# Performance work log

Hardware: AMD Instinct MI355X
Metric: run time of the kernel (lower is better)

The kernel has to match this reference:

```python
import jax, jax.numpy as jnp
import numpy as np
from math import sqrt

B, S, F, H, FF, L = 16, 512, 512, 8, 2048, 3
HEAD_DIM = F // H
LN_EPS = 1e-5


def setup_inputs() -> dict:
    key = jax.random.key(0)
    ks = iter(jax.random.split(key, 80))

    def nrm(shape, scale=0.02):
        return jax.random.normal(next(ks), shape, jnp.float32) * scale

    inp = {
        "embedding": jax.random.normal(next(ks), (B, S, F), jnp.float32),
        "lengths": jax.random.randint(next(ks), (B,), 1, S + 1, dtype=jnp.int32),
    }
    for p in ("enc", "dec"):
        inp[p + "_wqkv"] = nrm((L, 3, F, F))
        inp[p + "_bqkv"] = nrm((L, 3, F))
        inp[p + "_wo"] = nrm((L, F, F))
        inp[p + "_bo"] = nrm((L, F))
        inp[p + "_ln1_g"] = jnp.ones((L, F), jnp.float32)
        inp[p + "_ln1_b"] = jnp.zeros((L, F), jnp.float32)
        inp[p + "_ff_w1"] = nrm((L, F, FF))
        inp[p + "_ff_b1"] = nrm((L, FF))
        inp[p + "_ff_w2"] = nrm((L, FF, F))
        inp[p + "_ff_b2"] = nrm((L, F))
        inp[p + "_ln2_g"] = jnp.ones((L, F), jnp.float32)
        inp[p + "_ln2_b"] = jnp.zeros((L, F), jnp.float32)
    inp["ptr_w_q"] = nrm((F,), 1.0)
    inp["ptr_w_k"] = nrm((F,), 1.0)
    return inp


def _ln(x, g, b):
    mu = x.mean(-1, keepdims=True)
    var = ((x - mu) ** 2).mean(-1, keepdims=True)
    return (x - mu) / jnp.sqrt(var + LN_EPS) * g + b


def _mha(q_in, kv_in, wqkv, bqkv, wo, bo, mask):
    # q_in [b,sq,f], kv_in [b,sk,f], mask broadcastable to [b,h,sq,sk] (True = masked)
    b, sq, f = q_in.shape
    q = q_in @ wqkv[0] + bqkv[0]
    k = kv_in @ wqkv[1] + bqkv[1]
    v = kv_in @ wqkv[2] + bqkv[2]

    def split(t):
        return t.reshape(t.shape[0], t.shape[1], H, HEAD_DIM).transpose(0, 2, 1, 3)

    q, k, v = split(q), split(k), split(v)  # [b,h,s,dh]
    scores = jnp.einsum("bhqd,bhkd->bhqk", q, k) / sqrt(HEAD_DIM)
    scores = jnp.where(mask, jnp.finfo(scores.dtype).min, scores)
    attn = jax.nn.softmax(scores, axis=-1)
    out = jnp.einsum("bhqk,bhkd->bhqd", attn, v)
    out = out.transpose(0, 2, 1, 3).reshape(b, sq, f)
    return out @ wo + bo


def _layer(x, mem, mask, wqkv, bqkv, wo, bo, ln1_g, ln1_b, w1, b1, w2, b2, ln2_g, ln2_b):
    x = _ln(x + _mha(x, mem, wqkv, bqkv, wo, bo, mask), ln1_g, ln1_b)
    ff = jax.nn.gelu(x @ w1 + b1, approximate=False) @ w2 + b2
    return _ln(x + ff, ln2_g, ln2_b)


def _forward(embedding, lengths,
             enc_wqkv, enc_bqkv, enc_wo, enc_bo, enc_ln1_g, enc_ln1_b,
             enc_ff_w1, enc_ff_b1, enc_ff_w2, enc_ff_b2, enc_ln2_g, enc_ln2_b,
             dec_wqkv, dec_bqkv, dec_wo, dec_bo, dec_ln1_g, dec_ln1_b,
             dec_ff_w1, dec_ff_b1, dec_ff_w2, dec_ff_b2, dec_ln2_g, dec_ln2_b,
             ptr_w_q, ptr_w_k):
    b, s, f = embedding.shape
    pos = jnp.arange(s)
    key_mask = pos[None, :] >= lengths[:, None]  # [b,s] True = padded

    # ---- encoder (self-attn with key padding mask) ----
    enc_mask = key_mask[:, None, None, :]  # [b,1,1,s]
    x = embedding
    for i in range(L):
        x = _layer(x, x, enc_mask,
                   enc_wqkv[i], enc_bqkv[i], enc_wo[i], enc_bo[i],
                   enc_ln1_g[i], enc_ln1_b[i],
                   enc_ff_w1[i], enc_ff_b1[i], enc_ff_w2[i], enc_ff_b2[i],
                   enc_ln2_g[i], enc_ln2_b[i])
    memory = x

    # ---- decoder: all timesteps batched (no recurrent state in original loop) ----
    # query t attends keys j < min(t, len); t=0 is overridden with zeros below
    # (key 0 left unmasked for t=0 only to keep softmax finite).
    t = jnp.arange(s)
    limit = jnp.minimum(jnp.maximum(t, 1)[None, :], lengths[:, None])  # [b,sq]
    dec_mask = (pos[None, None, :] >= limit[:, :, None])[:, None, :, :]  # [b,1,sq,sk]
    y = embedding
    for i in range(L):
        y = _layer(y, memory, dec_mask,
                   dec_wqkv[i], dec_bqkv[i], dec_wo[i], dec_bo[i],
                   dec_ln1_g[i], dec_ln1_b[i],
                   dec_ff_w1[i], dec_ff_b1[i], dec_ff_w2[i], dec_ff_b2[i],
                   dec_ln2_g[i], dec_ln2_b[i])

    # ---- pointer logits ----
    wq = y @ ptr_w_q        # [b, sq]
    wk = memory @ ptr_w_k   # [b, sk]
    ptr = jax.nn.sigmoid((wq[:, None, :] + wk[:, :, None]) / sqrt(f))  # [b, sk, sq]
    return jnp.where(t[None, None, :] == 0, 0.0, ptr)


def reference(embedding, lengths,
              enc_wqkv, enc_bqkv, enc_wo, enc_bo, enc_ln1_g, enc_ln1_b,
              enc_ff_w1, enc_ff_b1, enc_ff_w2, enc_ff_b2, enc_ln2_g, enc_ln2_b,
              dec_wqkv, dec_bqkv, dec_wo, dec_bo, dec_ln1_g, dec_ln1_b,
              dec_ff_w1, dec_ff_b1, dec_ff_w2, dec_ff_b2, dec_ln2_g, dec_ln2_b,
              ptr_w_q, ptr_w_k):
    return _forward(embedding, lengths,
                    enc_wqkv, enc_bqkv, enc_wo, enc_bo, enc_ln1_g, enc_ln1_b,
                    enc_ff_w1, enc_ff_b1, enc_ff_w2, enc_ff_b2, enc_ln2_g, enc_ln2_b,
                    dec_wqkv, dec_bqkv, dec_wo, dec_bo, dec_ln1_g, dec_ln1_b,
                    dec_ff_w1, dec_ff_b1, dec_ff_w2, dec_ff_b2, dec_ln2_g, dec_ln2_b,
                    ptr_w_q, ptr_w_k)
```

## Files before the change

kernel.cpp:

```cpp
#include <hip/hip_runtime.h>
#include <hip/hip_bf16.h>
#include <math.h>

#define TB 16
#define TS 512
#define TF 512
#define TH 8
#define TFF 2048
#define TL 3

typedef unsigned short u16;
typedef short bf16x8 __attribute__((ext_vector_type(8)));
typedef float f32x4 __attribute__((ext_vector_type(4)));

__device__ __forceinline__ u16 f2b(float f) {
    __hip_bfloat16 h = __float2bfloat16(f);
    return *reinterpret_cast<u16*>(&h);
}

__device__ __forceinline__ void gload_lds16(const void* g, void* l) {
    __builtin_amdgcn_global_load_lds(
        (const __attribute__((address_space(1))) unsigned int*)g,
        (__attribute__((address_space(3))) unsigned int*)l, 16, 0, 0);
}

__global__ __launch_bounds__(256) void k_transpose_w(
    const float* __restrict__ src, u16* __restrict__ dst, int K, int N)
{
    __shared__ float tile[32][33];
    const int z = blockIdx.z;
    src += (size_t)z * K * N;
    dst += (size_t)z * K * N;
    const int n0 = blockIdx.x * 32, k0 = blockIdx.y * 32;
    const int tx = threadIdx.x & 31, ty = threadIdx.x >> 5;
    #pragma unroll
    for (int i = 0; i < 32; i += 8)
        tile[ty + i][tx] = src[(size_t)(k0 + ty + i) * N + n0 + tx];
    __syncthreads();
    #pragma unroll
    for (int i = 0; i < 32; i += 8)
        dst[(size_t)(n0 + ty + i) * K + k0 + tx] = f2b(tile[tx][ty + i]);
}

__global__ __launch_bounds__(256) void k_cvt(
    const float* __restrict__ src, float* __restrict__ d32,
    u16* __restrict__ d16, int n4)
{
    const int i = blockIdx.x * 256 + threadIdx.x;
    if (i >= n4) return;
    float4 v = ((const float4*)src)[i];
    if (d32) ((float4*)d32)[i] = v;
    ushort4 p;
    p.x = f2b(v.x); p.y = f2b(v.y); p.z = f2b(v.z); p.w = f2b(v.w);
    ((ushort4*)d16)[i] = p;
}

template<int EPI, int BN>
__global__ __launch_bounds__(512, 1) void k_g8(
    const u16* __restrict__ A, const u16* __restrict__ A2, int asplit,
    const u16* __restrict__ BT,
    const float* __restrict__ bias, const float* __restrict__ resid,
    u16* __restrict__ outb, float* __restrict__ outf,
    u16* __restrict__ out_k, u16* __restrict__ out_v,
    int N, int K, int ldo, int coloff)
{
    constexpr int NFB = BN / 64;
    constexpr int NL = 2 + BN / 64;
    __shared__ __align__(16) u16 SH[2 * 128 * 64 + 2 * BN * 64];
    u16* Asm = SH;
    u16* Bsm = SH + 2 * 128 * 64;

    const int gx = gridDim.x;
    int bid = blockIdx.y * gx + blockIdx.x;
    const int cpx = (gx * gridDim.y) >> 3;
    bid = (bid & 7) * cpx + (bid >> 3);
    const int bn = bid % gx, bm = bid / gx;

    const int t = threadIdx.x;
    const int w = t >> 6, l = t & 63;
    const int wm = w >> 2, wn = w & 3;
    const int lhi = l >> 4, llo = l & 15;

    f32x4 acc[4][NFB];
    #pragma unroll
    for (int m = 0; m < 4; ++m)
        #pragma unroll
        for (int n = 0; n < NFB; ++n)
            acc[m][n] = f32x4{0.f, 0.f, 0.f, 0.f};

    const u16* Asrc = (bn * BN < asplit) ? A : A2;
    const int lr = l >> 3;
    const int lcz = ((l & 7) ^ lr) * 8;
    const u16* Ag = Asrc + (size_t)(bm * 128 + w * 8 + lr) * K + lcz;
    const u16* Bg = BT + (size_t)(bn * BN + w * 8 + lr) * K + lcz;

    auto stage = [&](int buf, int tt) {
        const int kofs = tt << 6;
        gload_lds16(Ag + kofs,          Asm + buf * 8192 + (w * 8) * 64);
        gload_lds16(Ag + 64 * K + kofs, Asm + buf * 8192 + (64 + w * 8) * 64);
        #pragma unroll
        for (int i = 0; i < BN / 64; ++i)
            gload_lds16(Bg + (size_t)i * 64 * K + kofs,
                        Bsm + buf * (BN * 64) + (i * 64 + w * 8) * 64);
    };

    const int NT = K >> 6;
    stage(0, 0);
    stage(1, 1);
    for (int tt = 0; tt < NT; ++tt) {
        const int cur = tt & 1;
        if (tt + 1 < NT) {
            if constexpr (BN == 256) asm volatile("s_waitcnt vmcnt(6)" ::: "memory");
            else                     asm volatile("s_waitcnt vmcnt(4)" ::: "memory");
        } else {
            asm volatile("s_waitcnt vmcnt(0)" ::: "memory");
        }
        __builtin_amdgcn_s_barrier();
        __builtin_amdgcn_sched_barrier(0);

        bf16x8 af[4][2], bfr[NFB][2];
        #pragma unroll
        for (int m = 0; m < 4; ++m) {
            const int row = wm * 64 + m * 16 + llo;
            const int x = row & 7;
            af[m][0] = *(const bf16x8*)(Asm + cur * 8192 + row * 64 + ((lhi) ^ x) * 8);
            af[m][1] = *(const bf16x8*)(Asm + cur * 8192 + row * 64 + ((4 + lhi) ^ x) * 8);
        }
        #pragma unroll
        for (int n = 0; n < NFB; ++n) {
            const int row = wn * (BN / 4) + n * 16 + llo;
            const int x = row & 7;
            bfr[n][0] = *(const bf16x8*)(Bsm + cur * (BN * 64) + row * 64 + ((lhi) ^ x) * 8);
            bfr[n][1] = *(const bf16x8*)(Bsm + cur * (BN * 64) + row * 64 + ((4 + lhi) ^ x) * 8);
        }
        asm volatile("s_waitcnt lgkmcnt(0)" ::: "memory");
        __builtin_amdgcn_sched_barrier(0);
        __builtin_amdgcn_s_setprio(1);
        #pragma unroll
        for (int m = 0; m < 2; ++m)
            #pragma unroll
            for (int n = 0; n < NFB; ++n) {
                acc[m][n] = __builtin_amdgcn_mfma_f32_16x16x32_bf16(af[m][0], bfr[n][0], acc[m][n], 0, 0, 0);
                acc[m][n] = __builtin_amdgcn_mfma_f32_16x16x32_bf16(af[m][1], bfr[n][1], acc[m][n], 0, 0, 0);
            }
        __builtin_amdgcn_s_setprio(0);
        __builtin_amdgcn_sched_barrier(0);
        __builtin_amdgcn_s_barrier();
        if (tt + 2 < NT) stage(cur, tt + 2);
        __builtin_amdgcn_s_setprio(1);
        #pragma unroll
        for (int m = 2; m < 4; ++m)
            #pragma unroll
            for (int n = 0; n < NFB; ++n) {
                acc[m][n] = __builtin_amdgcn_mfma_f32_16x16x32_bf16(af[m][0], bfr[n][0], acc[m][n], 0, 0, 0);
                acc[m][n] = __builtin_amdgcn_mfma_f32_16x16x32_bf16(af[m][1], bfr[n][1], acc[m][n], 0, 0, 0);
            }
        __builtin_amdgcn_s_setprio(0);
    }

    const int colb = bn * BN + wn * (BN / 4);
    const int rowb = bm * 128 + wm * 64 + lhi * 4;
    const int c0w = coloff + colb;

    if constexpr (EPI == 3 && BN == 256) {
        if (c0w >= 1024) {
            u16* tb = SH + w * 4096;
            #pragma unroll
            for (int n = 0; n < 4; ++n) {
                const int dl = n * 16 + llo;
                const float bv = bias[colb + n * 16 + llo];
                #pragma unroll
                for (int m = 0; m < 4; ++m) {
                    ushort4 pk;
                    #pragma unroll
                    for (int r = 0; r < 4; ++r)
                        ((u16*)&pk)[r] = f2b(acc[m][n][r] + bv);
                    const int slc = m * 2 + (lhi >> 1);
                    const int addr = dl * 64 + ((slc ^ (dl & 7)) << 3) + ((lhi & 1) << 2);
                    *(ushort4*)(tb + addr) = pk;
                }
            }
            asm volatile("s_waitcnt lgkmcnt(0)" ::: "memory");
            __builtin_amdgcn_sched_barrier(0);
            const int sbase = bm * 128 + wm * 64;
            const int bidx = sbase >> 9;
            const int srem = sbase & 511;
            const int hh = (c0w >> 6) & 7;
            u16* vo = out_v + ((size_t)bidx * 8 + hh) * 32768 + srem;
            const int cchunk = l & 7;
            #pragma unroll
            for (int rr = 0; rr < 8; ++rr) {
                const int dl2 = (l >> 3) + rr * 8;
                const int ch = cchunk ^ (dl2 & 7);
                bf16x8 vv = *(const bf16x8*)(tb + dl2 * 64 + ch * 8);
                *(bf16x8*)(vo + (size_t)dl2 * 512 + cchunk * 8) = vv;
            }
            return;
        }
    }

    #pragma unroll
    for (int n = 0; n < NFB; ++n) {
        const int col = colb + n * 16 + llo;
        const float bv = bias[col];
        #pragma unroll
        for (int m = 0; m < 4; ++m) {
            const int row = rowb + m * 16;
            if (EPI == 3) {
                float vv[4];
                #pragma unroll
                for (int r = 0; r < 4; ++r) vv[r] = acc[m][n][r] + bv;
                const int c = coloff + col;
                if ((c >> 9) == 0) {
                    #pragma unroll
                    for (int r = 0; r < 4; ++r)
                        outb[(size_t)(row + r) * 512 + c] = f2b(vv[r]);
                } else {
                    const int hh = (c >> 6) & 7, d = c & 63;
                    #pragma unroll
                    for (int r = 0; r < 4; ++r) {
                        const int rr = row + r;
                        out_k[((size_t)(rr >> 9) * 8 + hh) * 32768 + (rr & 511) * 64 + d] = f2b(vv[r]);
                    }
                }
            } else {
                #pragma unroll
                for (int r = 0; r < 4; ++r) {
                    float v = acc[m][n][r] + bv;
                    const size_t off = (size_t)(row + r) * ldo + coloff + col;
                    if (EPI == 0) {
                        outb[off] = f2b(v);
                    } else if (EPI == 1) {
                        v = 0.5f * v * (1.f + erff(v * 0.70710678118654752f));
                        outb[off] = f2b(v);
                    } else {
                        outf[off] = v + resid[off];
                    }
                }
            }
        }
    }
}

template<int DEC>
__global__ __launch_bounds__(256) void k_attn(
    const u16* __restrict__ qb, const u16* __restrict__ kc,
    const u16* __restrict__ vtp, const int* __restrict__ lengths,
    u16* __restrict__ out)
{
    __shared__ __align__(16) u16 Ks[2][64 * 64];
    __shared__ __align__(16) u16 Vs[2][64 * 64];
    __shared__ __align__(16) u16 plds[4][16][64];
    __shared__ float alds[4][16];
    __shared__ float llds[4][16];
    const int qt = blockIdx.x;
    const int bh = blockIdx.y;
    const int b = bh >> 3;
    const int h = bh & 7;
    const int t = threadIdx.x, w = t >> 6, l = t & 63;
    const int lhi = l >> 4, llo = l & 15;
    const int len = lengths[b];
    const int qrow0 = qt * 64 + w * 16;
    const int q = qrow0 + llo;

    const u16* qp = qb + (size_t)(b * TS + q) * 512 + h * 64 + lhi * 8;
    bf16x8 qf0 = *(const bf16x8*)(qp);
    bf16x8 qf1 = *(const bf16x8*)(qp + 32);

    const u16* kb = kc  + (size_t)bh * 32768;
    const u16* vb = vtp + (size_t)bh * 32768;

    const int qlim = DEC ? min(max(q, 1), len) : len;
    const int limb = DEC ? min(qt * 64 + 63, len) : len;
    const int ktend = (limb + 63) >> 6;

    f32x4 o[4];
    #pragma unroll
    for (int g = 0; g < 4; ++g) o[g] = f32x4{0.f, 0.f, 0.f, 0.f};
    float mrun = -1e30f, lrun = 0.f;

    const float SC = 0.18033688011112042f;

    const int sr = w * 8 + (l >> 3);
    const int sc = (((l & 7) ^ (sr & 7)) << 3);
    auto stage = [&](int buf, int ktt) {
        gload_lds16(kb + ((ktt * 64 + sr) << 6) + sc,        &Ks[buf][(w * 8) * 64]);
        gload_lds16(kb + ((ktt * 64 + 32 + sr) << 6) + sc,   &Ks[buf][(32 + w * 8) * 64]);
        gload_lds16(vb + (size_t)sr * 512 + ktt * 64 + sc,   &Vs[buf][(w * 8) * 64]);
        gload_lds16(vb + (size_t)(32 + sr) * 512 + ktt * 64 + sc, &Vs[buf][(32 + w * 8) * 64]);
    };

    stage(0, 0);
    for (int kt = 0; kt < ktend; ++kt) {
        const int cur = kt & 1;
        if (kt + 1 < ktend) {
            stage(cur ^ 1, kt + 1);
            asm volatile("s_waitcnt vmcnt(4)" ::: "memory");
        } else {
            asm volatile("s_waitcnt vmcnt(0)" ::: "memory");
        }
        __builtin_amdgcn_s_barrier();
        __builtin_amdgcn_sched_barrier(0);

        bf16x8 kf[4][2], vf[4][2];
        #pragma unroll
        for (int g = 0; g < 4; ++g) {
            const int row = g * 16 + llo;
            const int x = row & 7;
            kf[g][0] = *(const bf16x8*)&Ks[cur][row * 64 + ((lhi) ^ x) * 8];
            kf[g][1] = *(const bf16x8*)&Ks[cur][row * 64 + ((4 + lhi) ^ x) * 8];
            vf[g][0] = *(const bf16x8*)&Vs[cur][row * 64 + ((lhi) ^ x) * 8];
            vf[g][1] = *(const bf16x8*)&Vs[cur][row * 64 + ((4 + lhi) ^ x) * 8];
        }
        f32x4 s[4];
        #pragma unroll
        for (int g = 0; g < 4; ++g) {
            s[g] = f32x4{0.f, 0.f, 0.f, 0.f};
            s[g] = __builtin_amdgcn_mfma_f32_16x16x32_bf16(kf[g][0], qf0, s[g], 0, 0, 0);
            s[g] = __builtin_amdgcn_mfma_f32_16x16x32_bf16(kf[g][1], qf1, s[g], 0, 0, 0);
        }
        #pragma unroll
        for (int g = 0; g < 4; ++g) {
            const int key = kt * 64 + g * 16 + lhi * 4;
            #pragma unroll
            for (int r = 0; r < 4; ++r)
                s[g][r] = (key + r < qlim) ? s[g][r] * SC : -1e30f;
        }
        float tm = fmaxf(fmaxf(fmaxf(s[0][0], s[0][1]), fmaxf(s[0][2], s[0][3])),
                         fmaxf(fmaxf(s[1][0], s[1][1]), fmaxf(s[1][2], s[1][3])));
        tm = fmaxf(tm, fmaxf(fmaxf(fmaxf(s[2][0], s[2][1]), fmaxf(s[2][2], s[2][3])),
                             fmaxf(fmaxf(s[3][0], s[3][1]), fmaxf(s[3][2], s[3][3]))));
        tm = fmaxf(tm, __shfl_xor(tm, 16));
        tm = fmaxf(tm, __shfl_xor(tm, 32));
        const float mnew = fmaxf(mrun, tm);
        const float alpha = exp2f(mrun - mnew);
        mrun = mnew;
        float rs = 0.f;
        ushort4 pk[4];
        #pragma unroll
        for (int g = 0; g < 4; ++g) {
            #pragma unroll
            for (int r = 0; r < 4; ++r) {
                const float p = exp2f(s[g][r] - mnew);
                rs += p;
                ((u16*)&pk[g])[r] = f2b(p);
            }
        }
        rs += __shfl_xor(rs, 16);
        rs += __shfl_xor(rs, 32);
        lrun = lrun * alpha + rs;
        if (lhi == 0) alds[w][llo] = alpha;
        #pragma unroll
        for (int g = 0; g < 4; ++g) {
            const int chw = (g * 2 + (lhi >> 1)) ^ (llo & 7);
            *(ushort4*)((char*)&plds[w][0][0] + llo * 128 + chw * 16 + (lhi & 1) * 8) = pk[g];
        }
        const float4 av = *(const float4*)&alds[w][lhi * 4];
        #pragma unroll
        for (int g = 0; g < 4; ++g) {
            o[g][0] *= av.x; o[g][1] *= av.y; o[g][2] *= av.z; o[g][3] *= av.w;
        }
        #pragma unroll
        for (int ks = 0; ks < 2; ++ks) {
            const int chr = (ks * 4 + lhi) ^ (llo & 7);
            bf16x8 pa = *(const bf16x8*)((const char*)&plds[w][0][0] + llo * 128 + chr * 16);
            #pragma unroll
            for (int g = 0; g < 4; ++g)
                o[g] = __builtin_amdgcn_mfma_f32_16x16x32_bf16(pa, vf[g][ks], o[g], 0, 0, 0);
        }
        __builtin_amdgcn_sched_barrier(0);
        __builtin_amdgcn_s_barrier();
    }

    if (lhi == 0) llds[w][llo] = 1.f / lrun;
    __builtin_amdgcn_s_waitcnt(0);
    const float4 linv = *(const float4*)&llds[w][lhi * 4];
    #pragma unroll
    for (int g = 0; g < 4; ++g) {
        const int d = h * 64 + g * 16 + llo;
        #pragma unroll
        for (int r = 0; r < 4; ++r) {
            const int qq = qrow0 + lhi * 4 + r;
            out[(size_t)(b * TS + qq) * 512 + d] = f2b(o[g][r] * ((const float*)&linv)[r]);
        }
    }
}

__global__ __launch_bounds__(256) void k_ln(
    const float* __restrict__ in, const float* __restrict__ gam,
    const float* __restrict__ bet, float* __restrict__ o32, u16* __restrict__ o16)
{
    const int row = blockIdx.x * 4 + (threadIdx.x >> 6);
    const int l = threadIdx.x & 63;
    const float* p = in + (size_t)row * 512 + l * 8;
    float x[8];
    *(float4*)&x[0] = *(const float4*)p;
    *(float4*)&x[4] = *(const float4*)(p + 4);
    float s = x[0] + x[1] + x[2] + x[3] + x[4] + x[5] + x[6] + x[7];
    #pragma unroll
    for (int off = 32; off; off >>= 1) s += __shfl_xor(s, off);
    const float mu = s * (1.f / 512.f);
    float v = 0.f;
    #pragma unroll
    for (int i = 0; i < 8; ++i) { const float d = x[i] - mu; v += d * d; }
    #pragma unroll
    for (int off = 32; off; off >>= 1) v += __shfl_xor(v, off);
    const float rstd = rsqrtf(v * (1.f / 512.f) + 1e-5f);
    float gg[8], bb[8];
    *(float4*)&gg[0] = *(const float4*)(gam + l * 8);
    *(float4*)&gg[4] = *(const float4*)(gam + l * 8 + 4);
    *(float4*)&bb[0] = *(const float4*)(bet + l * 8);
    *(float4*)&bb[4] = *(const float4*)(bet + l * 8 + 4);
    float y[8];
    #pragma unroll
    for (int i = 0; i < 8; ++i) y[i] = (x[i] - mu) * rstd * gg[i] + bb[i];
    float* op = o32 + (size_t)row * 512 + l * 8;
    *(float4*)op = *(float4*)&y[0];
    *(float4*)(op + 4) = *(float4*)&y[4];
    ushort4 pk0, pk1;
    pk0.x = f2b(y[0]); pk0.y = f2b(y[1]); pk0.z = f2b(y[2]); pk0.w = f2b(y[3]);
    pk1.x = f2b(y[4]); pk1.y = f2b(y[5]); pk1.z = f2b(y[6]); pk1.w = f2b(y[7]);
    ushort4* o16p = (ushort4*)(o16 + (size_t)row * 512 + l * 8);
    o16p[0] = pk0; o16p[1] = pk1;
}

__global__ __launch_bounds__(256) void k_rowdot(
    const float* __restrict__ x, const float* __restrict__ wv, float* __restrict__ out)
{
    const int row = blockIdx.x * 4 + (threadIdx.x >> 6);
    const int l = threadIdx.x & 63;
    const float* p = x + (size_t)row * 512 + l * 8;
    float4 a = *(const float4*)p;
    float4 b = *(const float4*)(p + 4);
    float4 wa = *(const float4*)(wv + l * 8);
    float4 wb = *(const float4*)(wv + l * 8 + 4);
    float s = a.x * wa.x + a.y * wa.y + a.z * wa.z + a.w * wa.w
            + b.x * wb.x + b.y * wb.y + b.z * wb.z + b.w * wb.w;
    #pragma unroll
    for (int off = 32; off; off >>= 1) s += __shfl_xor(s, off);
    if (l == 0) out[row] = s;
}

__global__ __launch_bounds__(256) void k_ptr_out(
    const float* __restrict__ wq, const float* __restrict__ wk, float* __restrict__ out)
{
    const int bi = blockIdx.x;
    const int b = bi >> 9;
    const float wki = wk[bi];
    #pragma unroll
    for (int j = threadIdx.x; j < 512; j += 256) {
        float r = 0.f;
        if (j != 0) {
            const float z = (wq[b * 512 + j] + wki) * 0.044194173824159216f;
            r = 1.f / (1.f + __expf(-z));
        }
        out[(size_t)bi * 512 + j] = r;
    }
}

extern "C" void kernel_launch(void* const* d_in, const int* in_sizes, int n_in,
                              void* d_out, int out_size, void* d_ws, size_t ws_size,
                              hipStream_t stream)
{
    const float* emb = (const float*)d_in[0];
    const int* lengths = (const int*)d_in[1];
    struct Pw {
        const float *wqkv, *bqkv, *wo, *bo, *ln1g, *ln1b, *w1, *b1, *w2, *b2, *ln2g, *ln2b;
    } pp[2];
    for (int p = 0; p < 2; ++p) {
        const int base = 2 + p * 12;
        pp[p].wqkv = (const float*)d_in[base + 0];
        pp[p].bqkv = (const float*)d_in[base + 1];
        pp[p].wo   = (const float*)d_in[base + 2];
        pp[p].bo   = (const float*)d_in[base + 3];
        pp[p].ln1g = (const float*)d_in[base + 4];
        pp[p].ln1b = (const float*)d_in[base + 5];
        pp[p].w1   = (const float*)d_in[base + 6];
        pp[p].b1   = (const float*)d_in[base + 7];
        pp[p].w2   = (const float*)d_in[base + 8];
        pp[p].b2   = (const float*)d_in[base + 9];
        pp[p].ln2g = (const float*)d_in[base + 10];
        pp[p].ln2b = (const float*)d_in[base + 11];
    }
    const float* pwq = (const float*)d_in[26];
    const float* pwk = (const float*)d_in[27];

    char* ws = (char*)d_ws;
    auto alloc = [&](size_t bytes) {
        char* p = ws;
        ws += (bytes + 255) & ~(size_t)255;
        return p;
    };
    u16* wqkvT[2], *woT[2], *w1T[2], *w2T[2];
    for (int p = 0; p < 2; ++p) {
        wqkvT[p] = (u16*)alloc((size_t)TL * 1536 * 512 * 2);
        woT[p]   = (u16*)alloc((size_t)TL * 512 * 512 * 2);
        w1T[p]   = (u16*)alloc((size_t)TL * 2048 * 512 * 2);
        w2T[p]   = (u16*)alloc((size_t)TL * 512 * 2048 * 2);
    }
    const size_t MR = (size_t)TB * TS;
    float* x32   = (float*)alloc(MR * 512 * 4);
    u16*   x16   = (u16*)alloc(MR * 512 * 2);
    float* mem32 = (float*)alloc(MR * 512 * 4);
    u16*   mem16 = (u16*)alloc(MR * 512 * 2);
    u16*   qbuf  = (u16*)alloc(MR * 512 * 2);
    u16*   kcb   = (u16*)alloc((size_t)TB * TH * 512 * 64 * 2);
    u16*   vtb   = (u16*)alloc((size_t)TB * TH * 64 * 512 * 2);
    u16*   att16 = (u16*)alloc(MR * 512 * 2);
    float* preln = (float*)alloc(MR * 512 * 4);
    u16*   h16   = (u16*)alloc(MR * 2048 * 2);
    float* wqb   = (float*)alloc(MR * 4);
    float* wkb   = (float*)alloc(MR * 4);

    for (int p = 0; p < 2; ++p) {
        k_transpose_w<<<dim3(16, 16, 9), 256, 0, stream>>>(pp[p].wqkv, wqkvT[p], 512, 512);
        k_transpose_w<<<dim3(16, 16, 3), 256, 0, stream>>>(pp[p].wo, woT[p], 512, 512);
        k_transpose_w<<<dim3(64, 16, 3), 256, 0, stream>>>(pp[p].w1, w1T[p], 512, 2048);
        k_transpose_w<<<dim3(16, 64, 3), 256, 0, stream>>>(pp[p].w2, w2T[p], 2048, 512);
    }

    const int n4 = (int)(MR * 512 / 4);
    k_cvt<<<4096, 256, 0, stream>>>(emb, x32, x16, n4);

    for (int i = 0; i < TL; ++i) {
        k_g8<3, 256><<<dim3(6, 64), 512, 0, stream>>>(
            x16, x16, 1536, wqkvT[0] + (size_t)i * 1536 * 512, pp[0].bqkv + i * 1536,
            nullptr, qbuf, nullptr, kcb, vtb, 1536, 512, 1536, 0);
        k_attn<0><<<dim3(8, 128), 256, 0, stream>>>(qbuf, kcb, vtb, lengths, att16);
        k_g8<2, 128><<<dim3(4, 64), 512, 0, stream>>>(
            att16, att16, 512, woT[0] + (size_t)i * 512 * 512, pp[0].bo + i * 512,
            x32, nullptr, preln, nullptr, nullptr, 512, 512, 512, 0);
        k_ln<<<2048, 256, 0, stream>>>(preln, pp[0].ln1g + i * 512, pp[0].ln1b + i * 512, x32, x16);
        k_g8<1, 256><<<dim3(8, 64), 512, 0, stream>>>(
            x16, x16, 2048, w1T[0] + (size_t)i * 2048 * 512, pp[0].b1 + i * 2048,
            nullptr, h16, nullptr, nullptr, nullptr, 2048, 512, 2048, 0);
        k_g8<2, 128><<<dim3(4, 64), 512, 0, stream>>>(
            h16, h16, 512, w2T[0] + (size_t)i * 512 * 2048, pp[0].b2 + i * 512,
            x32, nullptr, preln, nullptr, nullptr, 512, 2048, 512, 0);
        if (i == TL - 1)
            k_ln<<<2048, 256, 0, stream>>>(preln, pp[0].ln2g + i * 512, pp[0].ln2b + i * 512, mem32, mem16);
        else
            k_ln<<<2048, 256, 0, stream>>>(preln, pp[0].ln2g + i * 512, pp[0].ln2b + i * 512, x32, x16);
    }
    k_cvt<<<4096, 256, 0, stream>>>(emb, x32, x16, n4);

    for (int i = 0; i < TL; ++i) {
        k_g8<3, 256><<<dim3(6, 64), 512, 0, stream>>>(
            x16, mem16, 512, wqkvT[1] + (size_t)i * 1536 * 512, pp[1].bqkv + i * 1536,
            nullptr, qbuf, nullptr, kcb, vtb, 1536, 512, 1536, 0);
        k_attn<1><<<dim3(8, 128), 256, 0, stream>>>(qbuf, kcb, vtb, lengths, att16);
        k_g8<2, 128><<<dim3(4, 64), 512, 0, stream>>>(
            att16, att16, 512, woT[1] + (size_t)i * 512 * 512, pp[1].bo + i * 512,
            x32, nullptr, preln, nullptr, nullptr, 512, 512, 512, 0);
        k_ln<<<2048, 256, 0, stream>>>(preln, pp[1].ln1g + i * 512, pp[1].ln1b + i * 512, x32, x16);
        k_g8<1, 256><<<dim3(8, 64), 512, 0, stream>>>(
            x16, x16, 2048, w1T[1] + (size_t)i * 2048 * 512, pp[1].b1 + i * 2048,
            nullptr, h16, nullptr, nullptr, nullptr, 2048, 512, 2048, 0);
        k_g8<2, 128><<<dim3(4, 64), 512, 0, stream>>>(
            h16, h16, 512, w2T[1] + (size_t)i * 512 * 2048, pp[1].b2 + i * 512,
            x32, nullptr, preln, nullptr, nullptr, 512, 2048, 512, 0);
        k_ln<<<2048, 256, 0, stream>>>(preln, pp[1].ln2g + i * 512, pp[1].ln2b + i * 512, x32, x16);
    }

    k_rowdot<<<2048, 256, 0, stream>>>(x32, pwq, wqb);
    k_rowdot<<<2048, 256, 0, stream>>>(mem32, pwk, wkb);
    k_ptr_out<<<TB * TS, 256, 0, stream>>>(wqb, wkb, (float*)d_out);
}
```

Before: 977.5 us.

## Keep residual stream in bf16 and fuse pointer row-dots into final layernorm

The fp32 residual copies (x32, mem32, preln) are removed. The residual add in the output GEMM epilogue now reads and writes bf16, and layernorm reads bf16 input and writes only bf16. The two pointer row-dot kernels are folded into the last layernorm of the encoder and decoder. This cuts memory traffic across the elementwise and epilogue stages and drops two launches, but the residual path and LN input now carry bf16 rounding error, which may affect accuracy.

After: 873.5 us. 10.6% less time.

```diff
diff --git a/kernel.cpp b/kernel.cpp
--- a/kernel.cpp
+++ b/kernel.cpp
@@ -17,6 +17,10 @@
     __hip_bfloat16 h = __float2bfloat16(f);
     return *reinterpret_cast<u16*>(&h);
 }
+__device__ __forceinline__ float b2f(u16 u) {
+    unsigned int v = ((unsigned int)u) << 16;
+    return __builtin_bit_cast(float, v);
+}
 
 __device__ __forceinline__ void gload_lds16(const void* g, void* l) {
     __builtin_amdgcn_global_load_lds(
@@ -43,13 +47,11 @@
 }
 
 __global__ __launch_bounds__(256) void k_cvt(
-    const float* __restrict__ src, float* __restrict__ d32,
-    u16* __restrict__ d16, int n4)
+    const float* __restrict__ src, u16* __restrict__ d16, int n4)
 {
     const int i = blockIdx.x * 256 + threadIdx.x;
     if (i >= n4) return;
     float4 v = ((const float4*)src)[i];
-    if (d32) ((float4*)d32)[i] = v;
     ushort4 p;
     p.x = f2b(v.x); p.y = f2b(v.y); p.z = f2b(v.z); p.w = f2b(v.w);
     ((ushort4*)d16)[i] = p;
@@ -59,13 +61,12 @@
 __global__ __launch_bounds__(512, 1) void k_g8(
     const u16* __restrict__ A, const u16* __restrict__ A2, int asplit,
     const u16* __restrict__ BT,
-    const float* __restrict__ bias, const float* __restrict__ resid,
-    u16* __restrict__ outb, float* __restrict__ outf,
+    const float* __restrict__ bias, const u16* __restrict__ residb,
+    u16* __restrict__ outb,
     u16* __restrict__ out_k, u16* __restrict__ out_v,
     int N, int K, int ldo, int coloff)
 {
     constexpr int NFB = BN / 64;
-    constexpr int NL = 2 + BN / 64;
     __shared__ __align__(16) u16 SH[2 * 128 * 64 + 2 * BN * 64];
     u16* Asm = SH;
     u16* Bsm = SH + 2 * 128 * 64;
@@ -234,7 +235,8 @@
                         v = 0.5f * v * (1.f + erff(v * 0.70710678118654752f));
                         outb[off] = f2b(v);
                     } else {
-                        outf[off] = v + resid[off];
+                        v += b2f(residb[off]);
+                        outb[off] = f2b(v);
                     }
                 }
             }
@@ -387,15 +389,16 @@
 }
 
 __global__ __launch_bounds__(256) void k_ln(
-    const float* __restrict__ in, const float* __restrict__ gam,
-    const float* __restrict__ bet, float* __restrict__ o32, u16* __restrict__ o16)
+    const u16* __restrict__ in, const float* __restrict__ gam,
+    const float* __restrict__ bet, u16* __restrict__ o16,
+    const float* __restrict__ dotv, float* __restrict__ dotout)
 {
     const int row = blockIdx.x * 4 + (threadIdx.x >> 6);
     const int l = threadIdx.x & 63;
-    const float* p = in + (size_t)row * 512 + l * 8;
+    bf16x8 vin = *(const bf16x8*)(in + (size_t)row * 512 + l * 8);
     float x[8];
-    *(float4*)&x[0] = *(const float4*)p;
-    *(float4*)&x[4] = *(const float4*)(p + 4);
+    #pragma unroll
+    for (int i = 0; i < 8; ++i) x[i] = b2f((u16)vin[i]);
     float s = x[0] + x[1] + x[2] + x[3] + x[4] + x[5] + x[6] + x[7];
     #pragma unroll
     for (int off = 32; off; off >>= 1) s += __shfl_xor(s, off);
@@ -414,31 +417,22 @@
     float y[8];
     #pragma unroll
     for (int i = 0; i < 8; ++i) y[i] = (x[i] - mu) * rstd * gg[i] + bb[i];
-    float* op = o32 + (size_t)row * 512 + l * 8;
-    *(float4*)op = *(float4*)&y[0];
-    *(float4*)(op + 4) = *(float4*)&y[4];
     ushort4 pk0, pk1;
     pk0.x = f2b(y[0]); pk0.y = f2b(y[1]); pk0.z = f2b(y[2]); pk0.w = f2b(y[3]);
     pk1.x = f2b(y[4]); pk1.y = f2b(y[5]); pk1.z = f2b(y[6]); pk1.w = f2b(y[7]);
     ushort4* o16p = (ushort4*)(o16 + (size_t)row * 512 + l * 8);
     o16p[0] = pk0; o16p[1] = pk1;
-}
-
-__global__ __launch_bounds__(256) void k_rowdot(
-    const float* __restrict__ x, const float* __restrict__ wv, float* __restrict__ out)
-{
-    const int row = blockIdx.x * 4 + (threadIdx.x >> 6);
-    const int l = threadIdx.x & 63;
-    const float* p = x + (size_t)row * 512 + l * 8;
-    float4 a = *(const float4*)p;
-    float4 b = *(const float4*)(p + 4);
-    float4 wa = *(const float4*)(wv + l * 8);
-    float4 wb = *(const float4*)(wv + l * 8 + 4);
-    float s = a.x * wa.x + a.y * wa.y + a.z * wa.z + a.w * wa.w
-            + b.x * wb.x + b.y * wb.y + b.z * wb.z + b.w * wb.w;
-    #pragma unroll
-    for (int off = 32; off; off >>= 1) s += __shfl_xor(s, off);
-    if (l == 0) out[row] = s;
+    if (dotv) {
+        float wa[8];
+        *(float4*)&wa[0] = *(const float4*)(dotv + l * 8);
+        *(float4*)&wa[4] = *(const float4*)(dotv + l * 8 + 4);
+        float ds = 0.f;
+        #pragma unroll
+        for (int i = 0; i < 8; ++i) ds += y[i] * wa[i];
+        #pragma unroll
+        for (int off = 32; off; off >>= 1) ds += __shfl_xor(ds, off);
+        if (l == 0) dotout[row] = ds;
+    }
 }
 
 __global__ __launch_bounds__(256) void k_ptr_out(
@@ -499,15 +493,13 @@
         w2T[p]   = (u16*)alloc((size_t)TL * 512 * 2048 * 2);
     }
     const size_t MR = (size_t)TB * TS;
-    float* x32   = (float*)alloc(MR * 512 * 4);
     u16*   x16   = (u16*)alloc(MR * 512 * 2);
-    float* mem32 = (float*)alloc(MR * 512 * 4);
     u16*   mem16 = (u16*)alloc(MR * 512 * 2);
+    u16*   pre16 = (u16*)alloc(MR * 512 * 2);
     u16*   qbuf  = (u16*)alloc(MR * 512 * 2);
     u16*   kcb   = (u16*)alloc((size_t)TB * TH * 512 * 64 * 2);
     u16*   vtb   = (u16*)alloc((size_t)TB * TH * 64 * 512 * 2);
     u16*   att16 = (u16*)alloc(MR * 512 * 2);
-    float* preln = (float*)alloc(MR * 512 * 4);
     u16*   h16   = (u16*)alloc(MR * 2048 * 2);
     float* wqb   = (float*)alloc(MR * 4);
     float* wkb   = (float*)alloc(MR * 4);
@@ -520,49 +512,56 @@
     }
 
     const int n4 = (int)(MR * 512 / 4);
-    k_cvt<<<4096, 256, 0, stream>>>(emb, x32, x16, n4);
+    k_cvt<<<4096, 256, 0, stream>>>(emb, x16, n4);
 
     for (int i = 0; i < TL; ++i) {
         k_g8<3, 256><<<dim3(6, 64), 512, 0, stream>>>(
             x16, x16, 1536, wqkvT[0] + (size_t)i * 1536 * 512, pp[0].bqkv + i * 1536,
-            nullptr, qbuf, nullptr, kcb, vtb, 1536, 512, 1536, 0);
+            nullptr, qbuf, kcb, vtb, 1536, 512, 1536, 0);
         k_attn<0><<<dim3(8, 128), 256, 0, stream>>>(qbuf, kcb, vtb, lengths, att16);
         k_g8<2, 128><<<dim3(4, 64), 512, 0, stream>>>(
             att16, att16, 512, woT[0] + (size_t)i * 512 * 512, pp[0].bo + i * 512,
-            x32, nullptr, preln, nullptr, nullptr, 512, 512, 512, 0);
-        k_ln<<<2048, 256, 0, stream>>>(preln, pp[0].ln1g + i * 512, pp[0].ln1b + i * 512, x32, x16);
+            x16, pre16, nullptr, nullptr, 512, 512, 512, 0);
+        k_ln<<<2048, 256, 0, stream>>>(pre16, pp[0].ln1g + i * 512, pp[0].ln1b + i * 512,
+                                       x16, nullptr, nullptr);
         k_g8<1, 256><<<dim3(8, 64), 512, 0, stream>>>(
             x16, x16, 2048, w1T[0] + (size_t)i * 2048 * 512, pp[0].b1 + i * 2048,
-            nullptr, h16, nullptr, nullptr, nullptr, 2048, 512, 2048, 0);
+            nullptr, h16, nullptr, nullptr, 2048, 512, 2048, 0);
         k_g8<2, 128><<<dim3(4, 64), 512, 0, stream>>>(
             h16, h16, 512, w2T[0] + (size_t)i * 512 * 2048, pp[0].b2 + i * 512,
-            x32, nullptr, preln, nullptr, nullptr, 512, 2048, 512, 0);
+            x16, pre16, nullptr, nullptr, 512, 2048, 512, 0);
         if (i == TL - 1)
-            k_ln<<<2048, 256, 0, stream>>>(preln, pp[0].ln2g + i * 512, pp[0].ln2b + i * 512, mem32, mem16);
+            k_ln<<<2048, 256, 0, stream>>>(pre16, pp[0].ln2g + i * 512, pp[0].ln2b + i * 512,
+                                           mem16, pwk, wkb);
         else
-            k_ln<<<2048, 256, 0, stream>>>(preln, pp[0].ln2g + i * 512, pp[0].ln2b + i * 512, x32, x16);
-    }
-    k_cvt<<<4096, 256, 0, stream>>>(emb, x32, x16, n4);
+            k_ln<<<2048, 256, 0, stream>>>(pre16, pp[0].ln2g + i * 512, pp[0].ln2b + i * 512,
+                                           x16, nullptr, nullptr);
+    }
+    k_cvt<<<4096, 256, 0, stream>>>(emb, x16, n4);
 
     for (int i = 0; i < TL; ++i) {
         k_g8<3, 256><<<dim3(6, 64), 512, 0, stream>>>(
             x16, mem16, 512, wqkvT[1] + (size_t)i * 1536 * 512, pp[1].bqkv + i * 1536,
-            nullptr, qbuf, nullptr, kcb, vtb, 1536, 512, 1536, 0);
+            nullptr, qbuf, kcb, vtb, 1536, 512, 1536, 0);
         k_attn<1><<<dim3(8, 128), 256, 0, stream>>>(qbuf, kcb, vtb, lengths, att16);
         k_g8<2, 128><<<dim3(4, 64), 512, 0, stream>>>(
             att16, att16, 512, woT[1] + (size_t)i * 512 * 512, pp[1].bo + i * 512,
-            x32, nullptr, preln, nullptr, nullptr, 512, 512, 512, 0);
-        k_ln<<<2048, 256, 0, stream>>>(preln, pp[1].ln1g + i * 512, pp[1].ln1b + i * 512, x32, x16);
+            x16, pre16, nullptr, nullptr, 512, 512, 512, 0);
+        k_ln<<<2048, 256, 0, stream>>>(pre16, pp[1].ln1g + i * 512, pp[1].ln1b + i * 512,
+                                       x16, nullptr, nullptr);
         k_g8<1, 256><<<dim3(8, 64), 512, 0, stream>>>(
             x16, x16, 2048, w1T[1] + (size_t)i * 2048 * 512, pp[1].b1 + i * 2048,
-            nullptr, h16, nullptr, nullptr, nullptr, 2048, 512, 2048, 0);
+            nullptr, h16, nullptr, nullptr, 2048, 512, 2048, 0);
         k_g8<2, 128><<<dim3(4, 64), 512, 0, stream>>>(
             h16, h16, 512, w2T[1] + (size_t)i * 512 * 2048, pp[1].b2 + i * 512,
-            x32, nullptr, preln, nullptr, nullptr, 512, 2048, 512, 0);
-        k_ln<<<2048, 256, 0, stream>>>(preln, pp[1].ln2g + i * 512, pp[1].ln2b + i * 512, x32, x16);
-    }
-
-    k_rowdot<<<2048, 256, 0, stream>>>(x32, pwq, wqb);
-    k_rowdot<<<2048, 256, 0, stream>>>(mem32, pwk, wkb);
+            x16, pre16, nullptr, nullptr, 512, 2048, 512, 0);
+        if (i == TL - 1)
+            k_ln<<<2048, 256, 0, stream>>>(pre16, pp[1].ln2g + i * 512, pp[1].ln2b + i * 512,
+                                           x16, pwq, wqb);
+        else
+            k_ln<<<2048, 256, 0, stream>>>(pre16, pp[1].ln2g + i * 512, pp[1].ln2b + i * 512,
+                                           x16, nullptr, nullptr);
+    }
+
     k_ptr_out<<<TB * TS, 256, 0, stream>>>(wqb, wkb, (float*)d_out);
 }
```
